# Optimization experiments

Hardware: AMD Instinct MI355X
Metric: run time of the kernel (lower is better)

Reference implementation:

```python
import jax, jax.numpy as jnp
import numpy as np
import math

B, T, C, H = 4, 2048, 1024, 16
D = C // H  # head dim = 64
W_STD = 0.02


def setup_inputs() -> dict:
    key = jax.random.key(0)
    kx, kw, kb = jax.random.split(key, 3)
    x = jax.random.normal(kx, (B, T, C), dtype=jnp.float32)
    # Linear params stored as [in, 3*in] for x @ W; scaled like typical init
    w_qkv = jax.random.normal(kw, (C, 3 * C), dtype=jnp.float32) * W_STD
    b_qkv = jax.random.normal(kb, (3 * C,), dtype=jnp.float32) * W_STD
    return {"x": x, "w_qkv": w_qkv, "b_qkv": b_qkv}


def reference(x, w_qkv, b_qkv):
    # Fused QKV projection; torch splits as keys, queries, values (in that order)
    qkv = x @ w_qkv + b_qkv                      # [B, T, 3C]
    k, q, v = jnp.split(qkv, 3, axis=-1)          # each [B, T, C]

    def heads(t):  # [B, T, C] -> [B, H, T, D]
        return t.reshape(B, T, H, D).transpose(0, 2, 1, 3)

    k, q, v = heads(k), heads(q), heads(v)
    scale = 1.0 / math.sqrt(D)
    logits = jnp.einsum("bhqd,bhkd->bhqk", q, k) * scale  # [B, H, T, T]
    causal = jnp.tril(jnp.ones((T, T), dtype=bool))
    logits = jnp.where(causal, logits, -jnp.inf)
    probs = jax.nn.softmax(logits, axis=-1)
    y = jnp.einsum("bhqk,bhkd->bhqd", probs, v)   # [B, H, T, D]
    return y.transpose(0, 2, 1, 3).reshape(B, T, C)
```

## Files before the change

### kernel.cpp

```cpp
#include <hip/hip_runtime.h>
#include <hip/hip_bf16.h>

typedef unsigned short ushort_t;
typedef __attribute__((ext_vector_type(4))) short bf16x4_t;
typedef __attribute__((ext_vector_type(8))) short short8;
typedef __attribute__((ext_vector_type(4))) unsigned short ushort4_t;
typedef __attribute__((ext_vector_type(4))) float f32x4;
typedef __attribute__((ext_vector_type(2))) unsigned int uint2_t;
typedef __attribute__((ext_vector_type(4))) unsigned int uint4_t;

#define LOG2E 1.44269504088896340736f

__device__ __forceinline__ unsigned short f2bf(float f) {
    unsigned int u = __float_as_uint(f);
    u += 0x7fffu + ((u >> 16) & 1u);
    return (unsigned short)(u >> 16);
}

__device__ __forceinline__ unsigned int pk2bf(float a, float b) {
    union { __hip_bfloat162 h2; unsigned int u; } cvt;
    cvt.h2 = __float22bfloat162_rn(make_float2(a, b));
    return cvt.u;
}

__device__ __forceinline__ void gl_lds16(const ushort_t* g, ushort_t* l) {
    __builtin_amdgcn_global_load_lds(
        (const __attribute__((address_space(1))) unsigned int*)g,
        (__attribute__((address_space(3))) unsigned int*)l, 16, 0, 0);
}

__device__ __forceinline__ f32x4 mfma16(uint2_t a, uint2_t b, f32x4 c) {
    union { uint2_t u; bf16x4_t s; } ua, ub;
    ua.u = a; ub.u = b;
    return __builtin_amdgcn_mfma_f32_16x16x16bf16_1k(ua.s, ub.s, c, 0, 0, 0);
}

__device__ const signed char QT_TAB[24] =
    {15,15,7,14,14,13,13,6,12,12,11,11,5,10,10,9,9,4,8,8,3,2,1,0};
__device__ const signed char GR_TAB[24] =
    { 0, 1,2, 0, 1, 0, 1,2, 0, 1, 0, 1,2, 0, 1,0,1,2,0,1,2,2,2,2};

__global__ __launch_bounds__(256) void cvt_xw(
    const float* __restrict__ x, ushort_t* __restrict__ xb,
    const float* __restrict__ w, ushort_t* __restrict__ wt)
{
    __shared__ ushort_t Ts[64][40];
    const int bid = blockIdx.x;
    const int tid = threadIdx.x;
    if (bid < 4096) {
        const size_t i = ((size_t)bid * 256 + tid) * 8;
        const float4 a = *(const float4*)(x + i);
        const float4 b = *(const float4*)(x + i + 4);
        uint4_t o;
        o[0] = pk2bf(a.x, a.y); o[1] = pk2bf(a.z, a.w);
        o[2] = pk2bf(b.x, b.y); o[3] = pk2bf(b.z, b.w);
        *(uint4_t*)(xb + i) = o;
    } else {
        const int wb = bid - 4096;
        const int k0 = (wb & 31) * 32, n0 = (wb >> 5) * 64;
        const int kr = tid >> 3, nc = (tid & 7) * 8;
        const float* g = w + (size_t)(k0 + kr) * 3072 + n0 + nc;
        const float4 a = *(const float4*)g;
        const float4 b = *(const float4*)(g + 4);
        const float vals[8] = {a.x, a.y, a.z, a.w, b.x, b.y, b.z, b.w};
#pragma unroll
        for (int j = 0; j < 8; ++j) Ts[nc + j][kr] = f2bf(vals[j]);
        __syncthreads();
        const int nr = tid >> 2, kc = (tid & 3) * 8;
        const short8 v = *(const short8*)&Ts[nr][kc];
        *(short8*)(wt + (size_t)(n0 + nr) * 1024 + k0 + kc) = v;
    }
}

__global__ __launch_bounds__(256) void qkv_gemm(
    const ushort_t* __restrict__ xb, const ushort_t* __restrict__ wt,
    const float* __restrict__ bq,
    ushort_t* __restrict__ kws, ushort_t* __restrict__ qws,
    ushort_t* __restrict__ vws)
{
    __shared__ ushort_t As[3][128 * 32];
    __shared__ ushort_t Bs[3][128 * 32];

    const int tid  = threadIdx.x;
    const int m0   = blockIdx.x * 128;
    const int n0   = blockIdx.y * 128;
    const int wv   = tid >> 6;
    const int lane = tid & 63;
    const int qr   = lane & 15;
    const int quad = lane >> 4;
    const int wm   = (wv >> 1) * 64;
    const int wn   = (wv & 1) * 64;

    const int lr   = lane >> 2;
    const int csw  = (lane & 3) ^ ((lr >> 1) & 3);
    const ushort_t* gA = xb + (size_t)(m0 + wv*32 + lr) * 1024 + csw*8;
    const ushort_t* gB = wt + (size_t)(n0 + wv*32 + lr) * 1024 + csw*8;
    const int sdst = wv * 1024;

    const int swq = quad ^ ((qr >> 1) & 3);

    f32x4 acc[4][4];
#pragma unroll
    for (int i = 0; i < 4; ++i)
#pragma unroll
        for (int j = 0; j < 4; ++j) acc[i][j] = (f32x4){0.f, 0.f, 0.f, 0.f};

    gl_lds16(gA,             (ushort_t*)As + sdst);
    gl_lds16(gA + 16*1024,   (ushort_t*)As + sdst + 512);
    gl_lds16(gB,             (ushort_t*)Bs + sdst);
    gl_lds16(gB + 16*1024,   (ushort_t*)Bs + sdst + 512);
    gl_lds16(gA + 32,            (ushort_t*)As + 4096 + sdst);
    gl_lds16(gA + 32 + 16*1024,  (ushort_t*)As + 4096 + sdst + 512);
    gl_lds16(gB + 32,            (ushort_t*)Bs + 4096 + sdst);
    gl_lds16(gB + 32 + 16*1024,  (ushort_t*)Bs + 4096 + sdst + 512);

    int bufc = 0;
    for (int kt = 0; kt < 32; ++kt) {
        if (kt < 31) asm volatile("s_waitcnt vmcnt(4)" ::: "memory");
        else         asm volatile("s_waitcnt vmcnt(0)" ::: "memory");
        __builtin_amdgcn_s_barrier();
        __builtin_amdgcn_sched_barrier(0);

        const ushort_t* cA = (const ushort_t*)As + bufc * 4096;
        const ushort_t* cB = (const ushort_t*)Bs + bufc * 4096;
        short8 af[4], bfr[4];
#pragma unroll
        for (int i = 0; i < 4; ++i)
            af[i] = *(const short8*)&cA[(wm + i*16 + qr) * 32 + swq * 8];
#pragma unroll
        for (int j = 0; j < 4; ++j)
            bfr[j] = *(const short8*)&cB[(wn + j*16 + qr) * 32 + swq * 8];

        if (kt < 30) {
            int b2 = bufc + 2;
            if (b2 >= 3) b2 -= 3;
            const int k2 = (kt + 2) * 32;
            ushort_t* dA = (ushort_t*)As + b2 * 4096 + sdst;
            ushort_t* dB = (ushort_t*)Bs + b2 * 4096 + sdst;
            gl_lds16(gA + k2,            dA);
            gl_lds16(gA + k2 + 16*1024,  dA + 512);
            gl_lds16(gB + k2,            dB);
            gl_lds16(gB + k2 + 16*1024,  dB + 512);
        }

#pragma unroll
        for (int i = 0; i < 4; ++i)
#pragma unroll
            for (int j = 0; j < 4; ++j)
                acc[i][j] = __builtin_amdgcn_mfma_f32_16x16x32_bf16(
                    af[i], bfr[j], acc[i][j], 0, 0, 0);

        asm volatile("s_waitcnt lgkmcnt(0)" ::: "memory");
        bufc = (bufc == 2) ? 0 : bufc + 1;
    }

    const int nbase = n0 + wn;
    const int sec   = nbase >> 10;
    const int h     = (nbase & 1023) >> 6;

    if (sec == 2) {
#pragma unroll
        for (int j = 0; j < 4; ++j) {
            const float bias = bq[nbase + j*16 + qr];
            const int d = j*16 + qr;
#pragma unroll
            for (int i = 0; i < 4; ++i) {
                const int m  = m0 + wm + i*16 + quad*4;
                const int bb = m >> 11;
                const int tt = m & 2047;
                ushort4_t pk;
#pragma unroll
                for (int r = 0; r < 4; ++r) pk[r] = f2bf(acc[i][j][r] + bias);
                *(ushort4_t*)&vws[((size_t)(bb*16 + h)*64 + d)*2048 + tt] = pk;
            }
        }
    } else {
        ushort_t* __restrict__ dst = (sec == 0) ? kws : qws;
#pragma unroll
        for (int j = 0; j < 4; ++j) {
            const float bias = bq[nbase + j*16 + qr];
            const int d = j*16 + qr;
#pragma unroll
            for (int i = 0; i < 4; ++i) {
#pragma unroll
                for (int r = 0; r < 4; ++r) {
                    const int m  = m0 + wm + i*16 + quad*4 + r;
                    const int bb = m >> 11;
                    const int tt = m & 2047;
                    dst[(((size_t)(bb*16 + h)) * 2048 + tt) * 64 + d] =
                        f2bf(acc[i][j][r] + bias);
                }
            }
        }
    }
}


__global__ __launch_bounds__(512) void attn_fwd_split(
    const ushort_t* __restrict__ kws, const ushort_t* __restrict__ qws,
    const ushort_t* __restrict__ vws, float* __restrict__ out,
    float* __restrict__ pO1, float* __restrict__ pL)
{
    constexpr int LDK = 72;
    __shared__ ushort_t Ks[2][64 * LDK];
    __shared__ ushort_t Vs[2][64 * LDK];

    const int tid  = threadIdx.x;
    const int wv   = tid >> 6;
    const int lane = tid & 63;
    const int qr   = lane & 15;
    const int quad = lane >> 4;
    const int srow = tid >> 3;
    const int scol = (tid & 7) * 8;
    constexpr float SCL = 0.125f * LOG2E;
    constexpr float CB  = 8.0f;

    const int bid  = (int)blockIdx.x;
    const int item = bid >> 6;
    const int bh   = bid & 63;
    const int qt   = QT_TAB[item];
    const int gr   = GR_TAB[item];
    const size_t bhT = (size_t)bh * 2048;
    const ushort_t* kbase = kws + bhT * 64;
    const ushort_t* vbase = vws + (size_t)bh * 64 * 2048;
    const int b = bh >> 4, h = bh & 15;

    const int nt    = (gr == 2) ? (2*qt + 2) : (qt + 1);
    const int tile0 = (gr == 1) ? (qt + 1) : 0;
    const int q0    = qt * 128;
    const int base  = q0 + wv*16;
    const int qv0   = base + qr;
    const int row_max = base + 15;

    const ushort_t* qg0 = qws + (bhT + qv0) * 64;
    const short8 Qb00 = *(const short8*)(qg0 + quad*8);
    const short8 Qb01 = *(const short8*)(qg0 + 32 + quad*8);

    float l_s = 0.f;
    f32x4 Oacc[4];
#pragma unroll
    for (int dt = 0; dt < 4; ++dt) Oacc[dt] = (f32x4){0.f,0.f,0.f,0.f};

    short8 kv0, vv0;
    {
        const ushort_t* kg = kbase + (size_t)(tile0*64 + srow) * 64 + scol;
        const ushort_t* vg = vbase + (size_t)srow * 2048 + tile0*64 + scol;
        kv0 = *(const short8*)(kg);
        vv0 = *(const short8*)(vg);
    }
    *(short8*)&Ks[0][srow * LDK + scol] = kv0;
    *(short8*)&Vs[0][srow * LDK + scol] = vv0;
    __syncthreads();

    for (int t = 0; t < nt; ++t) {
        const int k0  = (tile0 + t) * 64;
        const int cur = t & 1;
        const bool more = (t + 1 < nt);
        if (more) {
            const ushort_t* kg = kbase + (size_t)(k0 + 64 + srow) * 64 + scol;
            const ushort_t* vg = vbase + (size_t)srow * 2048 + k0 + 64 + scol;
            kv0 = *(const short8*)(kg);
            vv0 = *(const short8*)(vg);
        }

        if (k0 <= row_max) {
            const ushort_t* Kc = Ks[cur];
            const ushort_t* Vc = Vs[cur];
            const bool diag = (k0 + 63 > base);

            uint2_t pks[4];
            float ps0 = 0.f;
#pragma unroll
            for (int t4 = 0; t4 < 4; ++t4) {
                const short8 kf0 = *(const short8*)&Kc[(t4*16 + qr)*LDK + quad*8];
                const short8 kf1 = *(const short8*)&Kc[(t4*16 + qr)*LDK + 32 + quad*8];
                f32x4 a = (f32x4){0.f,0.f,0.f,0.f};
                a = __builtin_amdgcn_mfma_f32_16x16x32_bf16(kf0, Qb00, a, 0,0,0);
                a = __builtin_amdgcn_mfma_f32_16x16x32_bf16(kf1, Qb01, a, 0,0,0);
                if (diag) {
#pragma unroll
                    for (int r = 0; r < 4; ++r) {
                        const int key = k0 + t4*16 + quad*4 + r;
                        if (key > qv0) a[r] = -INFINITY;
                    }
                }
                float p0[4];
#pragma unroll
                for (int r = 0; r < 4; ++r) {
                    p0[r] = exp2f(__builtin_fmaf(a[r], SCL, -CB));
                    ps0 += p0[r];
                }
                pks[t4][0] = pk2bf(p0[0], p0[1]);
                pks[t4][1] = pk2bf(p0[2], p0[3]);
            }
            l_s += ps0;

            __builtin_amdgcn_s_setprio(1);
#pragma unroll
            for (int dt = 0; dt < 4; ++dt) {
#pragma unroll
                for (int t4 = 0; t4 < 4; ++t4) {
                    const uint2_t vf = *(const uint2_t*)
                        &Vc[(dt*16 + qr)*LDK + t4*16 + quad*4];
                    Oacc[dt] = mfma16(pks[t4], vf, Oacc[dt]);
                }
            }
            __builtin_amdgcn_s_setprio(0);
        }

        if (more) {
            *(short8*)&Ks[cur ^ 1][srow * LDK + scol] = kv0;
            *(short8*)&Vs[cur ^ 1][srow * LDK + scol] = vv0;
        }
        __syncthreads();
    }

    float lf = l_s;
    lf += __shfl_xor(lf, 16);
    lf += __shfl_xor(lf, 32);

    if (gr == 2) {
#pragma unroll
        for (int r = 0; r < 4; ++r) {
            const float lr  = __shfl(lf, quad*4 + r);
            const float inv = 1.f / lr;
            const int q = q0 + wv*16 + quad*4 + r;
            float* o = out + ((size_t)(b*2048 + q)) * 1024 + h*64;
#pragma unroll
            for (int dt = 0; dt < 4; ++dt) o[dt*16 + qr] = Oacc[dt][r] * inv;
        }
    } else {
        const int qtidx = qt - 8;
        if (quad == 0)
            pL[((size_t)(gr*64 + bh)*8 + qtidx)*128 + wv*16 + qr] = lf;
        if (gr == 0) {
#pragma unroll
            for (int r = 0; r < 4; ++r) {
                const int q = q0 + wv*16 + quad*4 + r;
                float* o = out + ((size_t)(b*2048 + q)) * 1024 + h*64;
#pragma unroll
                for (int dt = 0; dt < 4; ++dt) o[dt*16 + qr] = Oacc[dt][r];
            }
        } else {
#pragma unroll
            for (int r = 0; r < 4; ++r) {
                const int ql = wv*16 + quad*4 + r;
                float* p = pO1 + (((size_t)bh*8 + qtidx)*128 + ql)*64;
#pragma unroll
                for (int dt = 0; dt < 4; ++dt) p[dt*16 + qr] = Oacc[dt][r];
            }
        }
    }
}

__global__ __launch_bounds__(256) void attn_combine(
    float* __restrict__ out, const float* __restrict__ pO1,
    const float* __restrict__ pL)
{
    const int bid   = (int)blockIdx.x;
    const int bh    = bid & 63;
    const int qtidx = bid >> 6;
    const int b = bh >> 4, h = bh & 15;
    const int q0 = (8 + qtidx) * 128;

    const int tid = threadIdx.x;
    const int row = tid >> 1;
    const int d0  = (tid & 1) * 32;

    const size_t li = ((size_t)bh*8 + qtidx)*128 + row;
    const float l0 = pL[li];
    const float l1 = pL[(size_t)64*8*128 + li];
    const float inv = 1.f / (l0 + l1);

    float4* ov = (float4*)(out + ((size_t)(b*2048 + q0 + row))*1024 + h*64 + d0);
    const float4* pv = (const float4*)(pO1 + (((size_t)bh*8 + qtidx)*128 + row)*64 + d0);
#pragma unroll
    for (int j = 0; j < 8; ++j) {
        const float4 a = ov[j];
        const float4 c = pv[j];
        ov[j] = make_float4((a.x + c.x)*inv, (a.y + c.y)*inv,
                            (a.z + c.z)*inv, (a.w + c.w)*inv);
    }
}

__global__ __launch_bounds__(512) void attn_fwd(
    const ushort_t* __restrict__ kws, const ushort_t* __restrict__ qws,
    const ushort_t* __restrict__ vws, float* __restrict__ out)
{
    constexpr int LDK = 72;
    __shared__ ushort_t Ks[2][64 * LDK];
    __shared__ ushort_t Vs[2][64 * LDK];

    const int tid  = threadIdx.x;
    const int wv   = tid >> 6;
    const int lane = tid & 63;
    const int qr   = lane & 15;
    const int quad = lane >> 4;
    const int srow = tid >> 3;
    const int scol = (tid & 7) * 8;
    constexpr float SCL = 0.125f * LOG2E;
    constexpr float CB  = 8.0f;

    const int bid = (int)blockIdx.x;
    const int qt  = 15 - (bid >> 6);
    const int bh  = bid & 63;
    const size_t bhT = (size_t)bh * 2048;
    const ushort_t* kbase = kws + bhT * 64;
    const ushort_t* vbase = vws + (size_t)bh * 64 * 2048;
    const int b = bh >> 4, h = bh & 15;

    const int q0 = qt * 128;
    const int base = q0 + wv*16;
    const int qv0 = base + qr;

    const ushort_t* qg0 = qws + (bhT + qv0) * 64;
    const short8 Qb00 = *(const short8*)(qg0 + quad*8);
    const short8 Qb01 = *(const short8*)(qg0 + 32 + quad*8);

    float l_s = 0.f;
    f32x4 Oacc[4];
#pragma unroll
    for (int dt = 0; dt < 4; ++dt) Oacc[dt] = (f32x4){0.f,0.f,0.f,0.f};

    const int nkt = 2*qt + 2;
    const int row_max = base + 15;

    short8 kv0, vv0;
    {
        const ushort_t* kg = kbase + (size_t)srow * 64 + scol;
        const ushort_t* vg = vbase + (size_t)srow * 2048 + scol;
        kv0 = *(const short8*)(kg);
        vv0 = *(const short8*)(vg);
    }
    *(short8*)&Ks[0][srow * LDK + scol] = kv0;
    *(short8*)&Vs[0][srow * LDK + scol] = vv0;
    __syncthreads();

    for (int kt = 0; kt < nkt; ++kt) {
        const int k0 = kt * 64;
        const int cur = kt & 1;
        const bool more = (kt + 1 < nkt);
        if (more) {
            const ushort_t* kg = kbase + (size_t)(k0 + 64 + srow) * 64 + scol;
            const ushort_t* vg = vbase + (size_t)srow * 2048 + k0 + 64 + scol;
            kv0 = *(const short8*)(kg);
            vv0 = *(const short8*)(vg);
        }

        if (k0 <= row_max) {
            const ushort_t* Kc = Ks[cur];
            const ushort_t* Vc = Vs[cur];
            const bool diag = (k0 + 63 > base);

            uint2_t pks[4];
            float ps0 = 0.f;
#pragma unroll
            for (int t4 = 0; t4 < 4; ++t4) {
                const short8 kf0 = *(const short8*)&Kc[(t4*16 + qr)*LDK + quad*8];
                const short8 kf1 = *(const short8*)&Kc[(t4*16 + qr)*LDK + 32 + quad*8];
                f32x4 a = (f32x4){0.f,0.f,0.f,0.f};
                a = __builtin_amdgcn_mfma_f32_16x16x32_bf16(kf0, Qb00, a, 0,0,0);
                a = __builtin_amdgcn_mfma_f32_16x16x32_bf16(kf1, Qb01, a, 0,0,0);
                if (diag) {
#pragma unroll
                    for (int r = 0; r < 4; ++r) {
                        const int key = k0 + t4*16 + quad*4 + r;
                        if (key > qv0) a[r] = -INFINITY;
                    }
                }
                float p0[4];
#pragma unroll
                for (int r = 0; r < 4; ++r) {
                    p0[r] = exp2f(__builtin_fmaf(a[r], SCL, -CB));
                    ps0 += p0[r];
                }
                pks[t4][0] = pk2bf(p0[0], p0[1]);
                pks[t4][1] = pk2bf(p0[2], p0[3]);
            }
            l_s += ps0;

            __builtin_amdgcn_s_setprio(1);
#pragma unroll
            for (int dt = 0; dt < 4; ++dt) {
#pragma unroll
                for (int t4 = 0; t4 < 4; ++t4) {
                    const uint2_t vf = *(const uint2_t*)
                        &Vc[(dt*16 + qr)*LDK + t4*16 + quad*4];
                    Oacc[dt] = mfma16(pks[t4], vf, Oacc[dt]);
                }
            }
            __builtin_amdgcn_s_setprio(0);
        }

        if (more) {
            *(short8*)&Ks[cur ^ 1][srow * LDK + scol] = kv0;
            *(short8*)&Vs[cur ^ 1][srow * LDK + scol] = vv0;
        }
        __syncthreads();
    }

    float lf = l_s;
    lf += __shfl_xor(lf, 16);
    lf += __shfl_xor(lf, 32);
#pragma unroll
    for (int r = 0; r < 4; ++r) {
        const float lr  = __shfl(lf, quad*4 + r);
        const float inv = 1.f / lr;
        const int q = q0 + wv*16 + quad*4 + r;
        float* o = out + ((size_t)(b*2048 + q)) * 1024 + h*64;
#pragma unroll
        for (int dt = 0; dt < 4; ++dt) o[dt*16 + qr] = Oacc[dt][r] * inv;
    }
}

extern "C" void kernel_launch(void* const* d_in, const int* in_sizes, int n_in,
                              void* d_out, int out_size, void* d_ws, size_t ws_size,
                              hipStream_t stream) {
    (void)in_sizes; (void)n_in; (void)out_size;
    const float* x  = (const float*)d_in[0];
    const float* w  = (const float*)d_in[1];
    const float* bq = (const float*)d_in[2];
    float* out = (float*)d_out;

    ushort_t* kws = (ushort_t*)d_ws;
    ushort_t* qws = kws + (size_t)8388608;
    ushort_t* vws = qws + (size_t)8388608;
    ushort_t* xb  = vws + (size_t)8388608;
    ushort_t* wt  = xb  + (size_t)8388608;

    float* pO1 = (float*)(wt + (size_t)8388608);
    float* pL  = pO1 + (size_t)64*8*128*64;
    const size_t ws_need = (size_t)5*16777216
                         + (size_t)64*8*128*64*4
                         + (size_t)2*64*8*128*4;

    cvt_xw<<<5632, 256, 0, stream>>>(x, xb, w, wt);
    qkv_gemm<<<dim3(64, 24), 256, 0, stream>>>(xb, wt, bq, kws, qws, vws);
    if (ws_size >= ws_need) {
        attn_fwd_split<<<1536, 512, 0, stream>>>(kws, qws, vws, out, pO1, pL);
        attn_combine<<<512, 256, 0, stream>>>(out, pO1, pL);
    } else {
        attn_fwd<<<1024, 512, 0, stream>>>(kws, qws, vws, out);
    }
}
```

Measured before the change: 236.8 us.

## Process two query sub-tiles per wave in split attention with 256-thread blocks

The split attention kernel now runs 4 waves of 256 threads instead of 8 waves, and each wave handles 32 query rows as two 16-row subtiles. Each K fragment and V fragment read from LDS is reused for two MFMAs, and each thread stages twice as much K/V data. The aim is to halve LDS fragment traffic per MFMA and to cut sync overhead per unit of work. In exchange it raises register pressure from doubled accumulators and P fragments, and it has fewer waves per block to hide latency.

```diff
diff --git a/kernel.cpp b/kernel.cpp
--- a/kernel.cpp
+++ b/kernel.cpp
@@ -195,11 +195,237 @@
     }
 }
 
-
-__global__ __launch_bounds__(512) void attn_fwd_split(
+__global__ __launch_bounds__(256) void attn_fwd_split(
     const ushort_t* __restrict__ kws, const ushort_t* __restrict__ qws,
     const ushort_t* __restrict__ vws, float* __restrict__ out,
     float* __restrict__ pO1, float* __restrict__ pL)
+{
+    constexpr int LDK = 72;
+    __shared__ ushort_t Ks[2][64 * LDK];
+    __shared__ ushort_t Vs[2][64 * LDK];
+
+    const int tid  = threadIdx.x;
+    const int wv   = tid >> 6;
+    const int lane = tid & 63;
+    const int qr   = lane & 15;
+    const int quad = lane >> 4;
+    const int srow = tid >> 2;
+    const int scol = (tid & 3) * 16;
+    constexpr float SCL = 0.125f * LOG2E;
+    constexpr float CB  = 8.0f;
+
+    const int bid  = (int)blockIdx.x;
+    const int item = bid >> 6;
+    const int bh   = bid & 63;
+    const int qt   = QT_TAB[item];
+    const int gr   = GR_TAB[item];
+    const size_t bhT = (size_t)bh * 2048;
+    const ushort_t* kbase = kws + bhT * 64;
+    const ushort_t* vbase = vws + (size_t)bh * 64 * 2048;
+    const int b = bh >> 4, h = bh & 15;
+
+    const int nt    = (gr == 2) ? (2*qt + 2) : (qt + 1);
+    const int tile0 = (gr == 1) ? (qt + 1) : 0;
+    const int q0    = qt * 128;
+    const int base  = q0 + wv*32;
+    const int qv0   = base + qr;
+    const int qv1   = qv0 + 16;
+    const int row_max = base + 31;
+
+    const ushort_t* qg0 = qws + (bhT + qv0) * 64;
+    const ushort_t* qg1 = qws + (bhT + qv1) * 64;
+    const short8 Qb00 = *(const short8*)(qg0 + quad*8);
+    const short8 Qb01 = *(const short8*)(qg0 + 32 + quad*8);
+    const short8 Qb10 = *(const short8*)(qg1 + quad*8);
+    const short8 Qb11 = *(const short8*)(qg1 + 32 + quad*8);
+
+    float l_s[2] = {0.f, 0.f};
+    f32x4 Oacc[2][4];
+#pragma unroll
+    for (int qs = 0; qs < 2; ++qs)
+#pragma unroll
+        for (int dt = 0; dt < 4; ++dt) Oacc[qs][dt] = (f32x4){0.f,0.f,0.f,0.f};
+
+    short8 kv0, kv1, vv0, vv1;
+    {
+        const ushort_t* kg = kbase + (size_t)(tile0*64 + srow) * 64 + scol;
+        const ushort_t* vg = vbase + (size_t)srow * 2048 + tile0*64 + scol;
+        kv0 = *(const short8*)(kg);     kv1 = *(const short8*)(kg + 8);
+        vv0 = *(const short8*)(vg);     vv1 = *(const short8*)(vg + 8);
+    }
+    *(short8*)&Ks[0][srow * LDK + scol]     = kv0;
+    *(short8*)&Ks[0][srow * LDK + scol + 8] = kv1;
+    *(short8*)&Vs[0][srow * LDK + scol]     = vv0;
+    *(short8*)&Vs[0][srow * LDK + scol + 8] = vv1;
+    __syncthreads();
+
+    for (int t = 0; t < nt; ++t) {
+        const int k0  = (tile0 + t) * 64;
+        const int cur = t & 1;
+        const bool more = (t + 1 < nt);
+        if (more) {
+            const ushort_t* kg = kbase + (size_t)(k0 + 64 + srow) * 64 + scol;
+            const ushort_t* vg = vbase + (size_t)srow * 2048 + k0 + 64 + scol;
+            kv0 = *(const short8*)(kg);   kv1 = *(const short8*)(kg + 8);
+            vv0 = *(const short8*)(vg);   vv1 = *(const short8*)(vg + 8);
+        }
+
+        if (k0 <= row_max) {
+            const ushort_t* Kc = Ks[cur];
+            const ushort_t* Vc = Vs[cur];
+            const bool diag = (k0 + 63 > base);
+
+            uint2_t pks[2][4];
+            float ps0 = 0.f, ps1 = 0.f;
+#pragma unroll
+            for (int t4 = 0; t4 < 4; ++t4) {
+                const short8 kf0 = *(const short8*)&Kc[(t4*16 + qr)*LDK + quad*8];
+                const short8 kf1 = *(const short8*)&Kc[(t4*16 + qr)*LDK + 32 + quad*8];
+                f32x4 a = (f32x4){0.f,0.f,0.f,0.f};
+                f32x4 bfr = (f32x4){0.f,0.f,0.f,0.f};
+                a   = __builtin_amdgcn_mfma_f32_16x16x32_bf16(kf0, Qb00, a, 0,0,0);
+                a   = __builtin_amdgcn_mfma_f32_16x16x32_bf16(kf1, Qb01, a, 0,0,0);
+                bfr = __builtin_amdgcn_mfma_f32_16x16x32_bf16(kf0, Qb10, bfr, 0,0,0);
+                bfr = __builtin_amdgcn_mfma_f32_16x16x32_bf16(kf1, Qb11, bfr, 0,0,0);
+                if (diag) {
+#pragma unroll
+                    for (int r = 0; r < 4; ++r) {
+                        const int key = k0 + t4*16 + quad*4 + r;
+                        if (key > qv0) a[r]   = -INFINITY;
+                        if (key > qv1) bfr[r] = -INFINITY;
+                    }
+                }
+                float p0[4], p1[4];
+#pragma unroll
+                for (int r = 0; r < 4; ++r) {
+                    p0[r] = exp2f(__builtin_fmaf(a[r],   SCL, -CB));
+                    p1[r] = exp2f(__builtin_fmaf(bfr[r], SCL, -CB));
+                    ps0 += p0[r];
+                    ps1 += p1[r];
+                }
+                pks[0][t4][0] = pk2bf(p0[0], p0[1]);
+                pks[0][t4][1] = pk2bf(p0[2], p0[3]);
+                pks[1][t4][0] = pk2bf(p1[0], p1[1]);
+                pks[1][t4][1] = pk2bf(p1[2], p1[3]);
+            }
+            l_s[0] += ps0;
+            l_s[1] += ps1;
+
+            __builtin_amdgcn_s_setprio(1);
+#pragma unroll
+            for (int dt = 0; dt < 4; ++dt) {
+#pragma unroll
+                for (int t4 = 0; t4 < 4; ++t4) {
+                    const uint2_t vf = *(const uint2_t*)
+                        &Vc[(dt*16 + qr)*LDK + t4*16 + quad*4];
+                    Oacc[0][dt] = mfma16(pks[0][t4], vf, Oacc[0][dt]);
+                    Oacc[1][dt] = mfma16(pks[1][t4], vf, Oacc[1][dt]);
+                }
+            }
+            __builtin_amdgcn_s_setprio(0);
+        }
+
+        if (more) {
+            *(short8*)&Ks[cur ^ 1][srow * LDK + scol]     = kv0;
+            *(short8*)&Ks[cur ^ 1][srow * LDK + scol + 8] = kv1;
+            *(short8*)&Vs[cur ^ 1][srow * LDK + scol]     = vv0;
+            *(short8*)&Vs[cur ^ 1][srow * LDK + scol + 8] = vv1;
+        }
+        __syncthreads();
+    }
+
+    float lf[2];
+#pragma unroll
+    for (int qs = 0; qs < 2; ++qs) {
+        float v = l_s[qs];
+        v += __shfl_xor(v, 16);
+        v += __shfl_xor(v, 32);
+        lf[qs] = v;
+    }
+
+    if (gr == 2) {
+#pragma unroll
+        for (int qs = 0; qs < 2; ++qs) {
+#pragma unroll
+            for (int r = 0; r < 4; ++r) {
+                const float lr  = __shfl(lf[qs], quad*4 + r);
+                const float inv = 1.f / lr;
+                const int q = q0 + wv*32 + qs*16 + quad*4 + r;
+                float* o = out + ((size_t)(b*2048 + q)) * 1024 + h*64;
+#pragma unroll
+                for (int dt = 0; dt < 4; ++dt)
+                    o[dt*16 + qr] = Oacc[qs][dt][r] * inv;
+            }
+        }
+    } else {
+        const int qtidx = qt - 8;
+#pragma unroll
+        for (int qs = 0; qs < 2; ++qs) {
+            if (quad == 0)
+                pL[((size_t)(gr*64 + bh)*8 + qtidx)*128 + wv*32 + qs*16 + qr]
+                    = lf[qs];
+        }
+        if (gr == 0) {
+#pragma unroll
+            for (int qs = 0; qs < 2; ++qs) {
+#pragma unroll
+                for (int r = 0; r < 4; ++r) {
+                    const int q = q0 + wv*32 + qs*16 + quad*4 + r;
+                    float* o = out + ((size_t)(b*2048 + q)) * 1024 + h*64;
+#pragma unroll
+                    for (int dt = 0; dt < 4; ++dt)
+                        o[dt*16 + qr] = Oacc[qs][dt][r];
+                }
+            }
+        } else {
+#pragma unroll
+            for (int qs = 0; qs < 2; ++qs) {
+#pragma unroll
+                for (int r = 0; r < 4; ++r) {
+                    const int ql = wv*32 + qs*16 + quad*4 + r;
+                    float* p = pO1 + (((size_t)bh*8 + qtidx)*128 + ql)*64;
+#pragma unroll
+                    for (int dt = 0; dt < 4; ++dt)
+                        p[dt*16 + qr] = Oacc[qs][dt][r];
+                }
+            }
+        }
+    }
+}
+
+__global__ __launch_bounds__(256) void attn_combine(
+    float* __restrict__ out, const float* __restrict__ pO1,
+    const float* __restrict__ pL)
+{
+    const int bid   = (int)blockIdx.x;
+    const int bh    = bid & 63;
+    const int qtidx = bid >> 6;
+    const int b = bh >> 4, h = bh & 15;
+    const int q0 = (8 + qtidx) * 128;
+
+    const int tid = threadIdx.x;
+    const int row = tid >> 1;
+    const int d0  = (tid & 1) * 32;
+
+    const size_t li = ((size_t)bh*8 + qtidx)*128 + row;
+    const float l0 = pL[li];
+    const float l1 = pL[(size_t)64*8*128 + li];
+    const float inv = 1.f / (l0 + l1);
+
+    float4* ov = (float4*)(out + ((size_t)(b*2048 + q0 + row))*1024 + h*64 + d0);
+    const float4* pv = (const float4*)(pO1 + (((size_t)bh*8 + qtidx)*128 + row)*64 + d0);
+#pragma unroll
+    for (int j = 0; j < 8; ++j) {
+        const float4 a = ov[j];
+        const float4 c = pv[j];
+        ov[j] = make_float4((a.x + c.x)*inv, (a.y + c.y)*inv,
+                            (a.z + c.z)*inv, (a.w + c.w)*inv);
+    }
+}
+
+__global__ __launch_bounds__(512) void attn_fwd(
+    const ushort_t* __restrict__ kws, const ushort_t* __restrict__ qws,
+    const ushort_t* __restrict__ vws, float* __restrict__ out)
 {
     constexpr int LDK = 72;
     __shared__ ushort_t Ks[2][64 * LDK];
@@ -215,192 +441,6 @@
     constexpr float SCL = 0.125f * LOG2E;
     constexpr float CB  = 8.0f;
 
-    const int bid  = (int)blockIdx.x;
-    const int item = bid >> 6;
-    const int bh   = bid & 63;
-    const int qt   = QT_TAB[item];
-    const int gr   = GR_TAB[item];
-    const size_t bhT = (size_t)bh * 2048;
-    const ushort_t* kbase = kws + bhT * 64;
-    const ushort_t* vbase = vws + (size_t)bh * 64 * 2048;
-    const int b = bh >> 4, h = bh & 15;
-
-    const int nt    = (gr == 2) ? (2*qt + 2) : (qt + 1);
-    const int tile0 = (gr == 1) ? (qt + 1) : 0;
-    const int q0    = qt * 128;
-    const int base  = q0 + wv*16;
-    const int qv0   = base + qr;
-    const int row_max = base + 15;
-
-    const ushort_t* qg0 = qws + (bhT + qv0) * 64;
-    const short8 Qb00 = *(const short8*)(qg0 + quad*8);
-    const short8 Qb01 = *(const short8*)(qg0 + 32 + quad*8);
-
-    float l_s = 0.f;
-    f32x4 Oacc[4];
-#pragma unroll
-    for (int dt = 0; dt < 4; ++dt) Oacc[dt] = (f32x4){0.f,0.f,0.f,0.f};
-
-    short8 kv0, vv0;
-    {
-        const ushort_t* kg = kbase + (size_t)(tile0*64 + srow) * 64 + scol;
-        const ushort_t* vg = vbase + (size_t)srow * 2048 + tile0*64 + scol;
-        kv0 = *(const short8*)(kg);
-        vv0 = *(const short8*)(vg);
-    }
-    *(short8*)&Ks[0][srow * LDK + scol] = kv0;
-    *(short8*)&Vs[0][srow * LDK + scol] = vv0;
-    __syncthreads();
-
-    for (int t = 0; t < nt; ++t) {
-        const int k0  = (tile0 + t) * 64;
-        const int cur = t & 1;
-        const bool more = (t + 1 < nt);
-        if (more) {
-            const ushort_t* kg = kbase + (size_t)(k0 + 64 + srow) * 64 + scol;
-            const ushort_t* vg = vbase + (size_t)srow * 2048 + k0 + 64 + scol;
-            kv0 = *(const short8*)(kg);
-            vv0 = *(const short8*)(vg);
-        }
-
-        if (k0 <= row_max) {
-            const ushort_t* Kc = Ks[cur];
-            const ushort_t* Vc = Vs[cur];
-            const bool diag = (k0 + 63 > base);
-
-            uint2_t pks[4];
-            float ps0 = 0.f;
-#pragma unroll
-            for (int t4 = 0; t4 < 4; ++t4) {
-                const short8 kf0 = *(const short8*)&Kc[(t4*16 + qr)*LDK + quad*8];
-                const short8 kf1 = *(const short8*)&Kc[(t4*16 + qr)*LDK + 32 + quad*8];
-                f32x4 a = (f32x4){0.f,0.f,0.f,0.f};
-                a = __builtin_amdgcn_mfma_f32_16x16x32_bf16(kf0, Qb00, a, 0,0,0);
-                a = __builtin_amdgcn_mfma_f32_16x16x32_bf16(kf1, Qb01, a, 0,0,0);
-                if (diag) {
-#pragma unroll
-                    for (int r = 0; r < 4; ++r) {
-                        const int key = k0 + t4*16 + quad*4 + r;
-                        if (key > qv0) a[r] = -INFINITY;
-                    }
-                }
-                float p0[4];
-#pragma unroll
-                for (int r = 0; r < 4; ++r) {
-                    p0[r] = exp2f(__builtin_fmaf(a[r], SCL, -CB));
-                    ps0 += p0[r];
-                }
-                pks[t4][0] = pk2bf(p0[0], p0[1]);
-                pks[t4][1] = pk2bf(p0[2], p0[3]);
-            }
-            l_s += ps0;
-
-            __builtin_amdgcn_s_setprio(1);
-#pragma unroll
-            for (int dt = 0; dt < 4; ++dt) {
-#pragma unroll
-                for (int t4 = 0; t4 < 4; ++t4) {
-                    const uint2_t vf = *(const uint2_t*)
-                        &Vc[(dt*16 + qr)*LDK + t4*16 + quad*4];
-                    Oacc[dt] = mfma16(pks[t4], vf, Oacc[dt]);
-                }
-            }
-            __builtin_amdgcn_s_setprio(0);
-        }
-
-        if (more) {
-            *(short8*)&Ks[cur ^ 1][srow * LDK + scol] = kv0;
-            *(short8*)&Vs[cur ^ 1][srow * LDK + scol] = vv0;
-        }
-        __syncthreads();
-    }
-
-    float lf = l_s;
-    lf += __shfl_xor(lf, 16);
-    lf += __shfl_xor(lf, 32);
-
-    if (gr == 2) {
-#pragma unroll
-        for (int r = 0; r < 4; ++r) {
-            const float lr  = __shfl(lf, quad*4 + r);
-            const float inv = 1.f / lr;
-            const int q = q0 + wv*16 + quad*4 + r;
-            float* o = out + ((size_t)(b*2048 + q)) * 1024 + h*64;
-#pragma unroll
-            for (int dt = 0; dt < 4; ++dt) o[dt*16 + qr] = Oacc[dt][r] * inv;
-        }
-    } else {
-        const int qtidx = qt - 8;
-        if (quad == 0)
-            pL[((size_t)(gr*64 + bh)*8 + qtidx)*128 + wv*16 + qr] = lf;
-        if (gr == 0) {
-#pragma unroll
-            for (int r = 0; r < 4; ++r) {
-                const int q = q0 + wv*16 + quad*4 + r;
-                float* o = out + ((size_t)(b*2048 + q)) * 1024 + h*64;
-#pragma unroll
-                for (int dt = 0; dt < 4; ++dt) o[dt*16 + qr] = Oacc[dt][r];
-            }
-        } else {
-#pragma unroll
-            for (int r = 0; r < 4; ++r) {
-                const int ql = wv*16 + quad*4 + r;
-                float* p = pO1 + (((size_t)bh*8 + qtidx)*128 + ql)*64;
-#pragma unroll
-                for (int dt = 0; dt < 4; ++dt) p[dt*16 + qr] = Oacc[dt][r];
-            }
-        }
-    }
-}
-
-__global__ __launch_bounds__(256) void attn_combine(
-    float* __restrict__ out, const float* __restrict__ pO1,
-    const float* __restrict__ pL)
-{
-    const int bid   = (int)blockIdx.x;
-    const int bh    = bid & 63;
-    const int qtidx = bid >> 6;
-    const int b = bh >> 4, h = bh & 15;
-    const int q0 = (8 + qtidx) * 128;
-
-    const int tid = threadIdx.x;
-    const int row = tid >> 1;
-    const int d0  = (tid & 1) * 32;
-
-    const size_t li = ((size_t)bh*8 + qtidx)*128 + row;
-    const float l0 = pL[li];
-    const float l1 = pL[(size_t)64*8*128 + li];
-    const float inv = 1.f / (l0 + l1);
-
-    float4* ov = (float4*)(out + ((size_t)(b*2048 + q0 + row))*1024 + h*64 + d0);
-    const float4* pv = (const float4*)(pO1 + (((size_t)bh*8 + qtidx)*128 + row)*64 + d0);
-#pragma unroll
-    for (int j = 0; j < 8; ++j) {
-        const float4 a = ov[j];
-        const float4 c = pv[j];
-        ov[j] = make_float4((a.x + c.x)*inv, (a.y + c.y)*inv,
-                            (a.z + c.z)*inv, (a.w + c.w)*inv);
-    }
-}
-
-__global__ __launch_bounds__(512) void attn_fwd(
-    const ushort_t* __restrict__ kws, const ushort_t* __restrict__ qws,
-    const ushort_t* __restrict__ vws, float* __restrict__ out)
-{
-    constexpr int LDK = 72;
-    __shared__ ushort_t Ks[2][64 * LDK];
-    __shared__ ushort_t Vs[2][64 * LDK];
-
-    const int tid  = threadIdx.x;
-    const int wv   = tid >> 6;
-    const int lane = tid & 63;
-    const int qr   = lane & 15;
-    const int quad = lane >> 4;
-    const int srow = tid >> 3;
-    const int scol = (tid & 7) * 8;
-    constexpr float SCL = 0.125f * LOG2E;
-    constexpr float CB  = 8.0f;
-
     const int bid = (int)blockIdx.x;
     const int qt  = 15 - (bid >> 6);
     const int bh  = bid & 63;
@@ -537,7 +577,7 @@
     cvt_xw<<<5632, 256, 0, stream>>>(x, xb, w, wt);
     qkv_gemm<<<dim3(64, 24), 256, 0, stream>>>(xb, wt, bq, kws, qws, vws);
     if (ws_size >= ws_need) {
-        attn_fwd_split<<<1536, 512, 0, stream>>>(kws, qws, vws, out, pO1, pL);
+        attn_fwd_split<<<1536, 256, 0, stream>>>(kws, qws, vws, out, pO1, pL);
         attn_combine<<<512, 256, 0, stream>>>(out, pO1, pL);
     } else {
         attn_fwd<<<1024, 512, 0, stream>>>(kws, qws, vws, out);
```

New measurement: 245.6 us. 1.04x slower.
